# Kernel optimization log

Hardware: AMD Instinct MI355X
Metric: run time of the kernel (lower is better)

The kernel has to match this reference:

```python
import jax, jax.numpy as jnp
import numpy as np

VOCAB = 100000
N_BLOCKS = 4
BLOCK_SIZES = [(25000, 64), (25000, 128), (25000, 256), (25000, 512)]
OUT_DIM = 512
B, L = 8, 2048


def setup_inputs() -> dict:
    key = jax.random.key(0)
    ks = jax.random.split(key, 2 * N_BLOCKS + 1)
    src = jax.random.randint(ks[0], (B, L), 0, VOCAB, dtype=jnp.int64 if jax.config.jax_enable_x64 else jnp.int32).astype(jnp.int32)
    # deterministic assignment: vocab idx -> block idx % 4, local row idx // 4
    idx = jnp.arange(VOCAB, dtype=jnp.int32)
    block_assignment = idx % N_BLOCKS
    local_assignment = idx // N_BLOCKS
    inp = {"src": src, "block_assignment": block_assignment, "local_assignment": local_assignment}
    for b, (num, size) in enumerate(BLOCK_SIZES):
        # embedding_initializer: normal_ (std=1); transformer_initializer: xavier_uniform_
        inp[f"block{b}"] = jax.random.normal(ks[1 + b], (num, size), dtype=jnp.float32)
        bound = np.sqrt(6.0 / (size + OUT_DIM))
        inp[f"trans{b}"] = jax.random.uniform(ks[1 + N_BLOCKS + b], (size, OUT_DIM), dtype=jnp.float32, minval=-bound, maxval=bound)
    return inp


def reference(src, block_assignment, local_assignment, block0, block1, block2, block3, trans0, trans1, trans2, trans3):
    blocks = [block0, block1, block2, block3]
    transformers = [trans0, trans1, trans2, trans3]
    ba = block_assignment[src]  # [B, L] which block each token routes to
    la = local_assignment[src]  # [B, L] row within that block's table
    out = jnp.zeros(src.shape + (OUT_DIM,), dtype=block0.dtype)
    for b in range(N_BLOCKS):
        tbl, tr = blocks[b], transformers[b]
        safe_la = jnp.clip(la, 0, tbl.shape[0] - 1)
        vec = tbl[safe_la]                      # [B, L, size_b] gather
        ob = jnp.einsum('bls,sd->bld', vec, tr)  # per-block transform
        out = jnp.where((ba == b)[..., None], ob, out)
    return out
```

## Files before the change

kernel.cpp:

```cpp
#include <hip/hip_runtime.h>
#include <stdint.h>


#define OUT_DIM 512
#define TOKBITS 14
#define TOKMASK ((1 << TOKBITS) - 1)
#define N_TOKENS_MAX 16384

typedef __attribute__((ext_vector_type(8))) short short8;
typedef __attribute__((ext_vector_type(4))) float floatx4;

__device__ __forceinline__ uint16_t f2bf(float f) {
    union { float f; uint32_t u; } x; x.f = f;
    uint32_t u = x.u + 0x7FFF + ((x.u >> 16) & 1);
    return (uint16_t)(u >> 16);
}

__global__ __launch_bounds__(256) void prep_bsw(
    const float* __restrict__ t0, const float* __restrict__ t1,
    const float* __restrict__ t2, const float* __restrict__ t3,
    uint16_t* __restrict__ bsw) {
    int gid = blockIdx.x * 256 + threadIdx.x;
    const float* tr; int S; int f; uint16_t* dst;
    if (gid < 4096)       { tr = t0; S = 64;  f = gid;         dst = bsw; }
    else if (gid < 12288) { tr = t1; S = 128; f = gid - 4096;  dst = bsw + 64 * 512; }
    else if (gid < 28672) { tr = t2; S = 256; f = gid - 12288; dst = bsw + (64 + 128) * 512; }
    else if (gid < 61440) { tr = t3; S = 512; f = gid - 28672; dst = bsw + (64 + 128 + 256) * 512; }
    else return;
    const int lane = f & 63, rest = f >> 6;
    const int ksteps = S >> 5;
    const int ks = rest & (ksteps - 1), ntile = rest / ksteps;
    const int quad = lane >> 4, nl = lane & 15;
    const int n = ntile * 16 + nl, k0 = ks * 32 + quad * 8;
    short8 v;
#pragma unroll
    for (int j = 0; j < 8; ++j) v[j] = (short)f2bf(tr[(k0 + j) * OUT_DIM + n]);
    *(short8*)(dst + (size_t)f * 8) = v;
}

__global__ __launch_bounds__(256) void scatter_kernel(
    const int* __restrict__ src, const int* __restrict__ ba, const int* __restrict__ la,
    int* __restrict__ counts, int* __restrict__ lists, int n_tokens, int stride) {
    __shared__ int lc[4], gbase[4];
    const int tid = (int)threadIdx.x;
    if (tid < 4) lc[tid] = 0;
    __syncthreads();
    const int t = blockIdx.x * 256 + tid;
    int b = 0, pos = 0, packed = 0;
    const bool active = (t < n_tokens);
    if (active) {
        int v = src[t];
        b = ba[v];
        int r = min(max(la[v], 0), 24999);
        packed = t | (r << TOKBITS);
        pos = atomicAdd(&lc[b], 1);
    }
    __syncthreads();
    if (tid < 4) gbase[tid] = atomicAdd(&counts[tid], lc[tid]);
    __syncthreads();
    if (active) lists[b * stride + gbase[b] + pos] = packed;
}

template <int S>
__device__ __forceinline__ void gemm_mfma_body(
    const float* __restrict__ tbl, const uint16_t* __restrict__ bsw,
    const int* __restrict__ list, const int* __restrict__ counts,
    float* __restrict__ out, uint16_t* lds, int b) {
    const int n = counts[b];
    const int base = (int)blockIdx.x * 32;
    if (base >= n) return;
    const int m = min(32, n - base);
    const int tid = (int)threadIdx.x;
    constexpr int SP = S + 8;
    constexpr int CH = S / 4;

    for (int i = tid; i < 32 * CH; i += 256) {
        const int row = i / CH, c = i & (CH - 1);
        float4 v = make_float4(0.f, 0.f, 0.f, 0.f);
        if (row < m) {
            const int r = list[base + row] >> TOKBITS;
            v = ((const float4*)(tbl + (size_t)r * S))[c];
        }
        const uint32_t lo = ((uint32_t)f2bf(v.y) << 16) | f2bf(v.x);
        const uint32_t hi = ((uint32_t)f2bf(v.w) << 16) | f2bf(v.z);
        *(uint2*)(lds + row * SP + c * 4) = make_uint2(lo, hi);
    }
    __syncthreads();

    const int wave = tid >> 6, lane = tid & 63;
    const int quad = lane >> 4, ml = lane & 15;
    constexpr int KS = S / 32;

    floatx4 acc[2][8];
#pragma unroll
    for (int mt = 0; mt < 2; ++mt)
#pragma unroll
        for (int nt = 0; nt < 8; ++nt) acc[mt][nt] = (floatx4)0.f;

    const short8* B = (const short8*)bsw;
#pragma unroll
    for (int ks = 0; ks < KS; ++ks) {
        const short8 a0 = *(const short8*)(lds + ml * SP + ks * 32 + quad * 8);
        const short8 a1 = *(const short8*)(lds + (16 + ml) * SP + ks * 32 + quad * 8);
#pragma unroll
        for (int nt = 0; nt < 8; ++nt) {
            const short8 bf = B[(size_t)((wave * 8 + nt) * KS + ks) * 64 + lane];
            acc[0][nt] = __builtin_amdgcn_mfma_f32_16x16x32_bf16(a0, bf, acc[0][nt], 0, 0, 0);
            acc[1][nt] = __builtin_amdgcn_mfma_f32_16x16x32_bf16(a1, bf, acc[1][nt], 0, 0, 0);
        }
    }

#pragma unroll
    for (int mt = 0; mt < 2; ++mt) {
#pragma unroll
        for (int r = 0; r < 4; ++r) {
            const int tokidx = mt * 16 + quad * 4 + r;
            if (tokidx < m) {
                const int t = list[base + tokidx] & TOKMASK;
                float* op = out + (size_t)t * OUT_DIM + wave * 128 + ml;
#pragma unroll
                for (int nt = 0; nt < 8; ++nt) op[nt * 16] = acc[mt][nt][r];
            }
        }
    }
}

__global__ __launch_bounds__(256) void gemm_mfma_all(
    const float* __restrict__ b0, const float* __restrict__ b1,
    const float* __restrict__ b2, const float* __restrict__ b3,
    const uint16_t* __restrict__ bsw,
    const int* __restrict__ lists, const int* __restrict__ counts,
    float* __restrict__ out, int stride) {
    extern __shared__ uint16_t lds[];
    switch ((int)blockIdx.y) {
        case 0: gemm_mfma_body<64 >(b0, bsw,                        lists + 0L * stride, counts, out, lds, 0); break;
        case 1: gemm_mfma_body<128>(b1, bsw + 64 * 512,             lists + 1L * stride, counts, out, lds, 1); break;
        case 2: gemm_mfma_body<256>(b2, bsw + (64 + 128) * 512,     lists + 2L * stride, counts, out, lds, 2); break;
        case 3: gemm_mfma_body<512>(b3, bsw + (64 + 128 + 256) * 512, lists + 3L * stride, counts, out, lds, 3); break;
    }
}

#define TOK 16
template <int S>
__device__ __forceinline__ void gemm_body(const float* __restrict__ tbl,
                                          const float* __restrict__ tr,
                                          const int* __restrict__ list,
                                          const int* __restrict__ counts,
                                          float* __restrict__ out,
                                          float* lvec, int b) {
    const int n = counts[b];
    const int base = (int)blockIdx.x * TOK;
    if (base >= n) return;
    const int m = min(TOK, n - base);
    const int tid = (int)threadIdx.x;
    const int nch = TOK * S / 4;
    for (int i = tid; i < nch; i += 256) {
        const int tok = i / (S / 4), c = i % (S / 4);
        float4 v = make_float4(0.f, 0.f, 0.f, 0.f);
        if (tok < m) {
            const int row = list[base + tok] >> TOKBITS;
            v = ((const float4*)(tbl + (size_t)row * S))[c];
        }
        ((float4*)lvec)[i] = v;
    }
    __syncthreads();
    float acc0[TOK], acc1[TOK];
#pragma unroll
    for (int tok = 0; tok < TOK; ++tok) { acc0[tok] = 0.f; acc1[tok] = 0.f; }
#pragma unroll 2
    for (int k = 0; k < S; k += 4) {
        float w00 = tr[(k + 0) * OUT_DIM + tid], w01 = tr[(k + 0) * OUT_DIM + tid + 256];
        float w10 = tr[(k + 1) * OUT_DIM + tid], w11 = tr[(k + 1) * OUT_DIM + tid + 256];
        float w20 = tr[(k + 2) * OUT_DIM + tid], w21 = tr[(k + 2) * OUT_DIM + tid + 256];
        float w30 = tr[(k + 3) * OUT_DIM + tid], w31 = tr[(k + 3) * OUT_DIM + tid + 256];
#pragma unroll
        for (int tok = 0; tok < TOK; ++tok) {
            float4 tv = *(const float4*)&lvec[tok * S + k];
            acc0[tok] += tv.x * w00 + tv.y * w10 + tv.z * w20 + tv.w * w30;
            acc1[tok] += tv.x * w01 + tv.y * w11 + tv.z * w21 + tv.w * w31;
        }
    }
    for (int tok = 0; tok < m; ++tok) {
        const int t = list[base + tok] & TOKMASK;
        out[(size_t)t * OUT_DIM + tid] = acc0[tok];
        out[(size_t)t * OUT_DIM + tid + 256] = acc1[tok];
    }
}

__global__ __launch_bounds__(256) void gemm_all(
    const float* __restrict__ b0, const float* __restrict__ b1,
    const float* __restrict__ b2, const float* __restrict__ b3,
    const float* __restrict__ t0, const float* __restrict__ t1,
    const float* __restrict__ t2, const float* __restrict__ t3,
    const int* __restrict__ lists, const int* __restrict__ counts,
    float* __restrict__ out, int stride) {
    extern __shared__ float lvec[];
    switch ((int)blockIdx.y) {
        case 0: gemm_body<64 >(b0, t0, lists + 0L * stride, counts, out, lvec, 0); break;
        case 1: gemm_body<128>(b1, t1, lists + 1L * stride, counts, out, lvec, 1); break;
        case 2: gemm_body<256>(b2, t2, lists + 2L * stride, counts, out, lvec, 2); break;
        case 3: gemm_body<512>(b3, t3, lists + 3L * stride, counts, out, lvec, 3); break;
    }
}

__global__ __launch_bounds__(256) void per_token_kernel(
    const int* __restrict__ src, const int* __restrict__ ba, const int* __restrict__ la,
    const float* __restrict__ b0, const float* __restrict__ b1,
    const float* __restrict__ b2, const float* __restrict__ b3,
    const float* __restrict__ t0, const float* __restrict__ t1,
    const float* __restrict__ t2, const float* __restrict__ t3,
    float* __restrict__ out) {
    __shared__ float lvec[OUT_DIM];
    const int t = (int)blockIdx.x, tid = (int)threadIdx.x;
    const int v = src[t];
    const int b = ba[v];
    int r = min(max(la[v], 0), 24999);
    const float* tbl; const float* tr; int S;
    switch (b) {
        case 0: tbl = b0; tr = t0; S = 64;  break;
        case 1: tbl = b1; tr = t1; S = 128; break;
        case 2: tbl = b2; tr = t2; S = 256; break;
        default: tbl = b3; tr = t3; S = 512; break;
    }
    if (tid < S / 4) ((float4*)lvec)[tid] = ((const float4*)(tbl + (size_t)r * S))[tid];
    __syncthreads();
    float acc0 = 0.f, acc1 = 0.f;
    for (int k = 0; k < S; ++k) {
        float x = lvec[k];
        acc0 += x * tr[k * OUT_DIM + tid];
        acc1 += x * tr[k * OUT_DIM + tid + 256];
    }
    out[(size_t)t * OUT_DIM + tid] = acc0;
    out[(size_t)t * OUT_DIM + tid + 256] = acc1;
}

extern "C" void kernel_launch(void* const* d_in, const int* in_sizes, int n_in,
                              void* d_out, int out_size, void* d_ws, size_t ws_size,
                              hipStream_t stream) {
    const int*   src = (const int*)d_in[0];
    const int*   ba  = (const int*)d_in[1];
    const int*   la  = (const int*)d_in[2];
    const float* b0  = (const float*)d_in[3];
    const float* t0  = (const float*)d_in[4];
    const float* b1  = (const float*)d_in[5];
    const float* t1  = (const float*)d_in[6];
    const float* b2  = (const float*)d_in[7];
    const float* t2  = (const float*)d_in[8];
    const float* b3  = (const float*)d_in[9];
    const float* t3  = (const float*)d_in[10];
    float* out = (float*)d_out;

    const int n_tokens = in_sizes[0];
    const size_t off_lists = 16;
    const size_t off_bsw   = off_lists + (size_t)4 * n_tokens * sizeof(int);
    const size_t bsw_bytes = (size_t)(64 + 128 + 256 + 512) * 512 * sizeof(uint16_t);
    const size_t need_full = off_bsw + bsw_bytes;
    const size_t need_fp32 = off_bsw;

    if (d_ws != nullptr && ws_size >= need_full) {
        int* counts   = (int*)d_ws;
        int* lists    = (int*)((char*)d_ws + off_lists);
        uint16_t* bsw = (uint16_t*)((char*)d_ws + off_bsw);
        hipMemsetAsync(d_ws, 0, 16, stream);
        prep_bsw<<<240, 256, 0, stream>>>(t0, t1, t2, t3, bsw);
        scatter_kernel<<<(n_tokens + 255) / 256, 256, 0, stream>>>(
            src, ba, la, counts, lists, n_tokens, n_tokens);
        const int groups = (n_tokens + 31) / 32;
        dim3 grid(groups, 4);
        gemm_mfma_all<<<grid, 256, 32 * (512 + 8) * sizeof(uint16_t), stream>>>(
            b0, b1, b2, b3, bsw, lists, counts, out, n_tokens);
    } else if (d_ws != nullptr && ws_size >= need_fp32) {
        int* counts = (int*)d_ws;
        int* lists  = (int*)((char*)d_ws + off_lists);
        hipMemsetAsync(d_ws, 0, 16, stream);
        scatter_kernel<<<(n_tokens + 255) / 256, 256, 0, stream>>>(
            src, ba, la, counts, lists, n_tokens, n_tokens);
        const int groups = (n_tokens + TOK - 1) / TOK;
        dim3 grid(groups, 4);
        gemm_all<<<grid, 256, TOK * OUT_DIM * sizeof(float), stream>>>(
            b0, b1, b2, b3, t0, t1, t2, t3, lists, counts, out, n_tokens);
    } else {
        per_token_kernel<<<n_tokens, 256, 0, stream>>>(
            src, ba, la, b0, b1, b2, b3, t0, t1, t2, t3, out);
    }
}
```

Measured before the change: 183.1 us.

## Flatten per-block token groups into one grid and split output columns across blocks

The GEMM launch no longer spans groups x 4 blocks, most of which exit early. It now uses a flat grid sized to the total group count plus 3, where each block finds its table from prefix sums of the per-table counts. A second grid dimension splits the 512 output columns into two halves, so each wave keeps 4 accumulator tiles instead of 8, and launch bounds request 4 blocks per CU. The memset of the counts is folded into prep_bsw and the LDS row pad grows to reduce bank conflicts. The cost is that each gathered row is converted twice, once per column half.

```diff
diff --git a/kernel.cpp b/kernel.cpp
--- a/kernel.cpp
+++ b/kernel.cpp
@@ -5,7 +5,6 @@
 #define OUT_DIM 512
 #define TOKBITS 14
 #define TOKMASK ((1 << TOKBITS) - 1)
-#define N_TOKENS_MAX 16384
 
 typedef __attribute__((ext_vector_type(8))) short short8;
 typedef __attribute__((ext_vector_type(4))) float floatx4;
@@ -19,7 +18,8 @@
 __global__ __launch_bounds__(256) void prep_bsw(
     const float* __restrict__ t0, const float* __restrict__ t1,
     const float* __restrict__ t2, const float* __restrict__ t3,
-    uint16_t* __restrict__ bsw) {
+    uint16_t* __restrict__ bsw, int* __restrict__ counts) {
+    if (blockIdx.x == 0 && threadIdx.x < 4) counts[threadIdx.x] = 0;
     int gid = blockIdx.x * 256 + threadIdx.x;
     const float* tr; int S; int f; uint16_t* dst;
     if (gid < 4096)       { tr = t0; S = 64;  f = gid;         dst = bsw; }
@@ -62,17 +62,16 @@
 }
 
 template <int S>
-__device__ __forceinline__ void gemm_mfma_body(
-    const float* __restrict__ tbl, const uint16_t* __restrict__ bsw,
-    const int* __restrict__ list, const int* __restrict__ counts,
-    float* __restrict__ out, uint16_t* lds, int b) {
-    const int n = counts[b];
-    const int base = (int)blockIdx.x * 32;
-    if (base >= n) return;
+__device__ __forceinline__ void gemm2_body(
+    const float* __restrict__ tbl, const uint16_t* __restrict__ bswb,
+    const int* __restrict__ list, int n, int g, int nhalf,
+    float* __restrict__ out, uint16_t* lds) {
+    const int base = g * 32;
     const int m = min(32, n - base);
     const int tid = (int)threadIdx.x;
-    constexpr int SP = S + 8;
+    constexpr int SP = S + 24;
     constexpr int CH = S / 4;
+    constexpr int KS = S / 32;
 
     for (int i = tid; i < 32 * CH; i += 256) {
         const int row = i / CH, c = i & (CH - 1);
@@ -89,22 +88,22 @@
 
     const int wave = tid >> 6, lane = tid & 63;
     const int quad = lane >> 4, ml = lane & 15;
-    constexpr int KS = S / 32;
-
-    floatx4 acc[2][8];
+    const int ntb = nhalf * 16 + wave * 4;
+
+    floatx4 acc[2][4];
 #pragma unroll
     for (int mt = 0; mt < 2; ++mt)
 #pragma unroll
-        for (int nt = 0; nt < 8; ++nt) acc[mt][nt] = (floatx4)0.f;
-
-    const short8* B = (const short8*)bsw;
+        for (int nt = 0; nt < 4; ++nt) acc[mt][nt] = (floatx4)0.f;
+
+    const short8* B = (const short8*)bswb;
 #pragma unroll
     for (int ks = 0; ks < KS; ++ks) {
         const short8 a0 = *(const short8*)(lds + ml * SP + ks * 32 + quad * 8);
         const short8 a1 = *(const short8*)(lds + (16 + ml) * SP + ks * 32 + quad * 8);
 #pragma unroll
-        for (int nt = 0; nt < 8; ++nt) {
-            const short8 bf = B[(size_t)((wave * 8 + nt) * KS + ks) * 64 + lane];
+        for (int nt = 0; nt < 4; ++nt) {
+            const short8 bf = B[(size_t)((ntb + nt) * KS + ks) * 64 + lane];
             acc[0][nt] = __builtin_amdgcn_mfma_f32_16x16x32_bf16(a0, bf, acc[0][nt], 0, 0, 0);
             acc[1][nt] = __builtin_amdgcn_mfma_f32_16x16x32_bf16(a1, bf, acc[1][nt], 0, 0, 0);
         }
@@ -117,26 +116,34 @@
             const int tokidx = mt * 16 + quad * 4 + r;
             if (tokidx < m) {
                 const int t = list[base + tokidx] & TOKMASK;
-                float* op = out + (size_t)t * OUT_DIM + wave * 128 + ml;
-#pragma unroll
-                for (int nt = 0; nt < 8; ++nt) op[nt * 16] = acc[mt][nt][r];
+                float* op = out + (size_t)t * OUT_DIM + nhalf * 256 + wave * 64 + ml;
+#pragma unroll
+                for (int nt = 0; nt < 4; ++nt) op[nt * 16] = acc[mt][nt][r];
             }
         }
     }
 }
 
-__global__ __launch_bounds__(256) void gemm_mfma_all(
+__global__ __launch_bounds__(256, 4) void gemm_mfma_v2(
     const float* __restrict__ b0, const float* __restrict__ b1,
     const float* __restrict__ b2, const float* __restrict__ b3,
     const uint16_t* __restrict__ bsw,
     const int* __restrict__ lists, const int* __restrict__ counts,
     float* __restrict__ out, int stride) {
     extern __shared__ uint16_t lds[];
-    switch ((int)blockIdx.y) {
-        case 0: gemm_mfma_body<64 >(b0, bsw,                        lists + 0L * stride, counts, out, lds, 0); break;
-        case 1: gemm_mfma_body<128>(b1, bsw + 64 * 512,             lists + 1L * stride, counts, out, lds, 1); break;
-        case 2: gemm_mfma_body<256>(b2, bsw + (64 + 128) * 512,     lists + 2L * stride, counts, out, lds, 2); break;
-        case 3: gemm_mfma_body<512>(b3, bsw + (64 + 128 + 256) * 512, lists + 3L * stride, counts, out, lds, 3); break;
+    const int c0 = counts[0], c1 = counts[1], c2 = counts[2], c3 = counts[3];
+    const int g0 = (c0 + 31) >> 5, g1 = (c1 + 31) >> 5, g2 = (c2 + 31) >> 5, g3 = (c3 + 31) >> 5;
+    const int flat = (int)blockIdx.x;
+    const int nhalf = (int)blockIdx.y;
+    if (flat >= g0 + g1 + g2 + g3) return;
+    if (flat < g0) {
+        gemm2_body<64 >(b0, bsw, lists + 0L * stride, c0, flat, nhalf, out, lds);
+    } else if (flat < g0 + g1) {
+        gemm2_body<128>(b1, bsw + 64 * 512, lists + 1L * stride, c1, flat - g0, nhalf, out, lds);
+    } else if (flat < g0 + g1 + g2) {
+        gemm2_body<256>(b2, bsw + (64 + 128) * 512, lists + 2L * stride, c2, flat - g0 - g1, nhalf, out, lds);
+    } else {
+        gemm2_body<512>(b3, bsw + (64 + 128 + 256) * 512, lists + 3L * stride, c3, flat - g0 - g1 - g2, nhalf, out, lds);
     }
 }
 
@@ -261,13 +268,12 @@
         int* counts   = (int*)d_ws;
         int* lists    = (int*)((char*)d_ws + off_lists);
         uint16_t* bsw = (uint16_t*)((char*)d_ws + off_bsw);
-        hipMemsetAsync(d_ws, 0, 16, stream);
-        prep_bsw<<<240, 256, 0, stream>>>(t0, t1, t2, t3, bsw);
+        prep_bsw<<<240, 256, 0, stream>>>(t0, t1, t2, t3, bsw, counts);
         scatter_kernel<<<(n_tokens + 255) / 256, 256, 0, stream>>>(
             src, ba, la, counts, lists, n_tokens, n_tokens);
-        const int groups = (n_tokens + 31) / 32;
-        dim3 grid(groups, 4);
-        gemm_mfma_all<<<grid, 256, 32 * (512 + 8) * sizeof(uint16_t), stream>>>(
+        const int gmax = (n_tokens + 31) / 32 + 3;
+        dim3 grid(gmax, 2);
+        gemm_mfma_v2<<<grid, 256, 32 * (512 + 24) * sizeof(uint16_t), stream>>>(
             b0, b1, b2, b3, bsw, lists, counts, out, n_tokens);
     } else if (d_ws != nullptr && ws_size >= need_fp32) {
         int* counts = (int*)d_ws;
```

Result: faster. 166.3 us (-9.2%).
